# Optimization experiments

Hardware: AMD Instinct MI355X
Metric: run time of the kernel (lower is better)

Reference implementation:

```python
import jax, jax.numpy as jnp
import numpy as np

B, L, D, H, M = 2, 4096, 1024, 16, 256
DH = D // H
EPS = 1e-6
LN_EPS = 1e-5


def setup_inputs() -> dict:
    key = jax.random.key(0)
    ks = jax.random.split(key, 6)
    inp = {
        "x": jax.random.normal(ks[0], (B, L, D), jnp.float32),
        "Wq": jax.random.normal(ks[1], (D, D), jnp.float32) * (D ** -0.5),
        "Wk": jax.random.normal(ks[2], (D, D), jnp.float32) * (D ** -0.5),
        "Wv": jax.random.normal(ks[3], (D, D), jnp.float32) * (D ** -0.5),
        "Wo": jax.random.normal(ks[4], (D, D), jnp.float32) * (D ** -0.5),
        "proj": jax.random.normal(ks[5], (H, M, DH), jnp.float32),
        "ln_g": jnp.ones((D,), jnp.float32),
        "ln_b": jnp.zeros((D,), jnp.float32),
        "scale_factor": 2,
    }
    return inp


def _heads(t, W):
    b, l, _ = t.shape
    return (t @ W).reshape(b, l, H, DH).transpose(0, 2, 1, 3)  # bhld


def _favor_features(u, proj):
    # u: [B,H,L,DH] already scaled by d_head**-0.25; proj: [H,M,DH]
    dash = jnp.einsum("bhld,hmd->bhlm", u, proj)
    diag = 0.5 * jnp.sum(u * u, axis=-1, keepdims=True)  # [B,H,L,1]
    stab = jnp.max(dash, axis=-1, keepdims=True)
    return jnp.exp(dash - diag - stab) * (M ** -0.5)  # [B,H,L,M]


def reference(x, Wq, Wk, Wv, Wo, proj, ln_g, ln_b, scale_factor):
    b, l, d = x.shape
    # nearest-neighbor upsample along sequence (F.interpolate default mode)
    up = jnp.repeat(x, scale_factor, axis=1)  # [B, L*s, D]

    scale = DH ** -0.25
    q = _heads(up, Wq) * scale   # [B,H,Lq,DH]
    k = _heads(x, Wk) * scale    # [B,H,L,DH]
    v = _heads(x, Wv)            # [B,H,L,DH]

    qf = _favor_features(q, proj)  # [B,H,Lq,M]
    kf = _favor_features(k, proj)  # [B,H,L,M]

    kv = jnp.einsum("bhlm,bhld->bhmd", kf, v)          # [B,H,M,DH]
    k_sum = jnp.sum(kf, axis=2)                          # [B,H,M]
    z = 1.0 / (jnp.einsum("bhlm,bhm->bhl", qf, k_sum) + EPS)
    attn = jnp.einsum("bhlm,bhmd->bhld", qf, kv) * z[..., None]

    lq = attn.shape[2]
    y = attn.transpose(0, 2, 1, 3).reshape(b, lq, d) @ Wo
    y = jax.nn.gelu(y, approximate=False)

    mu = jnp.mean(y, axis=-1, keepdims=True)
    var = jnp.mean((y - mu) ** 2, axis=-1, keepdims=True)
    return (y - mu) * jax.lax.rsqrt(var + LN_EPS) * ln_g + ln_b
```

## Files before the change

kernel.cpp:

```cpp
#include <hip/hip_runtime.h>

static constexpr int kB  = 2;
static constexpr int kL  = 4096;
static constexpr int kD  = 1024;
static constexpr int kH  = 16;
static constexpr int kDH = 64;
static constexpr int kM  = 256;
static constexpr int kN  = kB * kL;
static constexpr float kScale    = 0.35355339059327373f;
static constexpr float kInvSqrtM = 0.0625f;
static constexpr float kEps   = 1e-6f;
static constexpr float kLnEps = 1e-5f;

typedef __attribute__((ext_vector_type(8))) short short8;
typedef __attribute__((ext_vector_type(4))) float f32x4;

__device__ __forceinline__ float bf2f(unsigned short h) {
  union { unsigned int u; float f; } c;
  c.u = ((unsigned int)h) << 16;
  return c.f;
}
__device__ __forceinline__ unsigned short f2bf(float f) {
  union { float f; unsigned int u; } c;
  c.f = f;
  unsigned int u = c.u;
  u += 0x7fffu + ((u >> 16) & 1u);
  return (unsigned short)(u >> 16);
}

__device__ __forceinline__ void gload_lds16(const unsigned short* g,
                                            unsigned short* l) {
  __builtin_amdgcn_global_load_lds(
      (const __attribute__((address_space(1))) unsigned int*)g,
      (__attribute__((address_space(3))) unsigned int*)l, 16, 0, 0);
}

__global__ __launch_bounds__(256) void cast_bf16_kernel(
    const float* __restrict__ in, unsigned short* __restrict__ out)
{
  const int i = blockIdx.x * 256 + threadIdx.x;
  float4 v = ((const float4*)in)[i];
  ushort4 o;
  o.x = f2bf(v.x); o.y = f2bf(v.y); o.z = f2bf(v.z); o.w = f2bf(v.w);
  ((ushort4*)out)[i] = o;
}

__global__ __launch_bounds__(256) void transpose_cast_kernel(
    const float* __restrict__ W, unsigned short* __restrict__ WT)
{
  __shared__ float tile[32][33];
  const int n0 = blockIdx.x * 32, k0 = blockIdx.y * 32;
  const int t = threadIdx.x, kk = t >> 5, nn = t & 31;
#pragma unroll
  for (int i = 0; i < 4; ++i)
    tile[kk + i * 8][nn] = W[(size_t)(k0 + kk + i * 8) * kD + n0 + nn];
  __syncthreads();
#pragma unroll
  for (int i = 0; i < 4; ++i)
    WT[(size_t)(n0 + kk + i * 8) * kD + k0 + nn] = f2bf(tile[nn][kk + i * 8]);
}

template <int OUT_MODE>
__global__ __launch_bounds__(256) void gemm_mfma(
    const unsigned short* __restrict__ A, const unsigned short* __restrict__ BT,
    void* __restrict__ Cout, float alpha)
{
  __shared__ unsigned short As[128 * 32];
  __shared__ unsigned short Bs[128 * 32];
  __shared__ unsigned short Tbuf[OUT_MODE == 2 ? 64 * 136 : 1];
  const int tid = threadIdx.x, lane = tid & 63, w = tid >> 6;
  const int q = lane >> 4, c = lane & 15;
  const int wr = (w >> 1) * 64, wc = (w & 1) * 64;
  const int row0 = blockIdx.y * 128, col0 = blockIdx.x * 128;
  const int lrow = lane >> 2, lcol = (lane & 3) * 8;

  f32x4 acc[4][4];
#pragma unroll
  for (int i = 0; i < 4; ++i)
#pragma unroll
    for (int j = 0; j < 4; ++j) acc[i][j] = (f32x4)0.f;

  for (int k0 = 0; k0 < kD; k0 += 32) {
#pragma unroll
    for (int i = 0; i < 2; ++i) {
      const int r0 = w * 32 + i * 16;
      gload_lds16(&A[(size_t)(row0 + r0 + lrow) * kD + k0 + lcol], &As[r0 * 32]);
      gload_lds16(&BT[(size_t)(col0 + r0 + lrow) * kD + k0 + lcol], &Bs[r0 * 32]);
    }
    __syncthreads();
    short8 av[4], bv[4];
#pragma unroll
    for (int i = 0; i < 4; ++i)
      av[i] = *(const short8*)&As[(wr + i * 16 + c) * 32 + q * 8];
#pragma unroll
    for (int j = 0; j < 4; ++j)
      bv[j] = *(const short8*)&Bs[(wc + j * 16 + c) * 32 + q * 8];
#pragma unroll
    for (int i = 0; i < 4; ++i)
#pragma unroll
      for (int j = 0; j < 4; ++j)
        acc[i][j] = __builtin_amdgcn_mfma_f32_16x16x32_bf16(
            av[i], bv[j], acc[i][j], 0, 0, 0);
    __syncthreads();
  }

  if (OUT_MODE != 2) {
#pragma unroll
    for (int i = 0; i < 4; ++i)
#pragma unroll
      for (int j = 0; j < 4; ++j)
#pragma unroll
        for (int r = 0; r < 4; ++r) {
          const int row = row0 + wr + i * 16 + q * 4 + r;
          const int col = col0 + wc + j * 16 + c;
          const float v = alpha * acc[i][j][r];
          if (OUT_MODE == 1)
            ((unsigned short*)Cout)[(size_t)row * kD + col] = f2bf(v);
          else
            ((float*)Cout)[(size_t)row * kD + col] = v;
        }
  } else {
    const int bq = row0 >> 12, l0 = row0 & 4095;
#pragma unroll
    for (int hh = 0; hh < 2; ++hh) {
      if ((w & 1) == hh) {
#pragma unroll
        for (int i = 0; i < 4; ++i)
#pragma unroll
          for (int j = 0; j < 4; ++j) {
            ushort4 o;
            o.x = f2bf(acc[i][j][0]); o.y = f2bf(acc[i][j][1]);
            o.z = f2bf(acc[i][j][2]); o.w = f2bf(acc[i][j][3]);
            *(ushort4*)&Tbuf[(j * 16 + c) * 136 + wr + i * 16 + q * 4] = o;
          }
      }
      __syncthreads();
      {
        const int dl = tid >> 2, seg = tid & 3;
        const size_t dst =
            ((size_t)(bq * 1024 + col0 + hh * 64 + dl)) * (size_t)kL +
            l0 + seg * 32;
        uint4* gp = (uint4*)((unsigned short*)Cout + dst);
        const unsigned short* sp = &Tbuf[dl * 136 + seg * 32];
#pragma unroll
        for (int u = 0; u < 4; ++u) gp[u] = *(const uint4*)&sp[u * 8];
      }
      __syncthreads();
    }
  }
}

template <int TRANS>
__global__ __launch_bounds__(256) void favor_mfma(
    const unsigned short* __restrict__ U, const unsigned short* __restrict__ projb,
    unsigned short* __restrict__ F)
{
  __shared__ unsigned short Us[128 * 72];
  __shared__ unsigned short Ps[256 * 72];
  __shared__ float diagp[256];
  __shared__ float diag[128];
  unsigned short* Tbuf = Us;
  const int bh = blockIdx.x, b = bh >> 4, h = bh & 15;
  const int l0 = blockIdx.y * 128;
  const int tid = threadIdx.x, lane = tid & 63, w = tid >> 6;
  const int q = lane >> 4, c = lane & 15;
  const int wr = w * 32;

#pragma unroll
  for (int it = 0; it < 4; ++it) {
    int idx = it * 256 + tid;
    int row = idx >> 3, col8 = idx & 7;
    *(uint4*)&Us[row * 72 + col8 * 8] =
        *(const uint4*)&U[((size_t)(b * kL + l0 + row)) * kD + h * kDH + col8 * 8];
  }
#pragma unroll
  for (int it = 0; it < 8; ++it) {
    int idx = it * 256 + tid;
    int row = idx >> 3, col8 = idx & 7;
    *(uint4*)&Ps[row * 72 + col8 * 8] =
        *(const uint4*)&projb[((size_t)(h * kM + row)) * kDH + col8 * 8];
  }
  __syncthreads();

  {
    int row = tid & 127, half = tid >> 7;
    const unsigned short* ur = &Us[row * 72 + half * 32];
    float s = 0.f;
#pragma unroll
    for (int d8 = 0; d8 < 4; ++d8) {
      uint4 raw = *(const uint4*)&ur[d8 * 8];
      const unsigned short* us = (const unsigned short*)&raw;
#pragma unroll
      for (int j = 0; j < 8; ++j) { float v = bf2f(us[j]); s = fmaf(v, v, s); }
    }
    diagp[half * 128 + row] = s;
  }

  f32x4 acc[2][16];
#pragma unroll
  for (int i = 0; i < 2; ++i)
#pragma unroll
    for (int j = 0; j < 16; ++j) acc[i][j] = (f32x4)0.f;

#pragma unroll
  for (int ks = 0; ks < 2; ++ks) {
    short8 av[2];
#pragma unroll
    for (int i = 0; i < 2; ++i)
      av[i] = *(const short8*)&Us[(wr + i * 16 + c) * 72 + ks * 32 + q * 8];
#pragma unroll
    for (int jb = 0; jb < 2; ++jb) {
      short8 bv[8];
#pragma unroll
      for (int jl = 0; jl < 8; ++jl)
        bv[jl] = *(const short8*)&Ps[((jb * 8 + jl) * 16 + c) * 72 + ks * 32 + q * 8];
#pragma unroll
      for (int jl = 0; jl < 8; ++jl)
#pragma unroll
        for (int i = 0; i < 2; ++i)
          acc[i][jb * 8 + jl] = __builtin_amdgcn_mfma_f32_16x16x32_bf16(
              av[i], bv[jl], acc[i][jb * 8 + jl], 0, 0, 0);
    }
  }

  __syncthreads();
  if (tid < 128) diag[tid] = 0.5f * (diagp[tid] + diagp[128 + tid]);
  __syncthreads();

#pragma unroll
  for (int i = 0; i < 2; ++i)
#pragma unroll
    for (int r = 0; r < 4; ++r) {
      const int lrow = wr + i * 16 + q * 4 + r;
      float mx = -3.4e38f;
#pragma unroll
      for (int j = 0; j < 16; ++j) mx = fmaxf(mx, acc[i][j][r]);
      mx = fmaxf(mx, __shfl_xor(mx, 1, 64));
      mx = fmaxf(mx, __shfl_xor(mx, 2, 64));
      mx = fmaxf(mx, __shfl_xor(mx, 4, 64));
      mx = fmaxf(mx, __shfl_xor(mx, 8, 64));
      const float base = diag[lrow] + mx;
      if (TRANS == 0) {
        const size_t gbase = ((size_t)bh * kL + (l0 + lrow)) * kM;
#pragma unroll
        for (int j = 0; j < 16; ++j)
          F[gbase + j * 16 + c] = f2bf(__expf(acc[i][j][r] - base) * kInvSqrtM);
      } else {
#pragma unroll
        for (int j = 0; j < 16; ++j)
          acc[i][j][r] = __expf(acc[i][j][r] - base) * kInvSqrtM;
      }
    }

  if (TRANS == 1) {
#pragma unroll
    for (int mc = 0; mc < 4; ++mc) {
      __syncthreads();
#pragma unroll
      for (int jl = 0; jl < 4; ++jl) {
        const int jj = mc * 4 + jl;
#pragma unroll
        for (int i = 0; i < 2; ++i) {
          ushort4 o;
          o.x = f2bf(acc[i][jj][0]); o.y = f2bf(acc[i][jj][1]);
          o.z = f2bf(acc[i][jj][2]); o.w = f2bf(acc[i][jj][3]);
          *(ushort4*)&Tbuf[(jl * 16 + c) * 136 + wr + i * 16 + q * 4] = o;
        }
      }
      __syncthreads();
#pragma unroll
      for (int it = 0; it < 4; ++it) {
        int idx = it * 256 + tid;
        int row = idx >> 4, col8 = idx & 15;
        *(uint4*)&F[((size_t)(bh * kM + mc * 64 + row)) * (size_t)kL +
                    l0 + col8 * 8] = *(const uint4*)&Tbuf[row * 136 + col8 * 8];
      }
    }
  }
}

__global__ __launch_bounds__(256) void kv_mfma(
    const unsigned short* __restrict__ KFT, const unsigned short* __restrict__ VT,
    float* __restrict__ KVP, float* __restrict__ KSP)
{
  __shared__ unsigned short As[128 * 40];
  __shared__ unsigned short Bs[64 * 40];
  const int bh = blockIdx.x, mtile = blockIdx.y, split = blockIdx.z;
  const int tid = threadIdx.x, lane = tid & 63, w = tid >> 6;
  const int q = lane >> 4, c = lane & 15;
  const int l0 = split * 512;
  const unsigned short* Abase = KFT + ((size_t)(bh * kM + mtile * 128)) * kL + l0;
  const unsigned short* Bbase = VT + ((size_t)(bh * kDH)) * kL + l0;

  f32x4 acc[2][4];
#pragma unroll
  for (int i = 0; i < 2; ++i)
#pragma unroll
    for (int j = 0; j < 4; ++j) acc[i][j] = (f32x4)0.f;
  float ksr[2] = {0.f, 0.f};

  for (int k0 = 0; k0 < 512; k0 += 32) {
    __syncthreads();
#pragma unroll
    for (int it = 0; it < 2; ++it) {
      int idx = it * 256 + tid;
      int row = idx >> 2, c8 = (idx & 3) * 8;
      *(uint4*)&As[row * 40 + c8] = *(const uint4*)&Abase[(size_t)row * kL + k0 + c8];
    }
    {
      int row = tid >> 2, c8 = (tid & 3) * 8;
      *(uint4*)&Bs[row * 40 + c8] = *(const uint4*)&Bbase[(size_t)row * kL + k0 + c8];
    }
    __syncthreads();
    short8 av[2], bv[4];
#pragma unroll
    for (int i = 0; i < 2; ++i) {
      av[i] = *(const short8*)&As[(w * 32 + i * 16 + c) * 40 + q * 8];
#pragma unroll
      for (int e = 0; e < 8; ++e) ksr[i] += bf2f((unsigned short)av[i][e]);
    }
#pragma unroll
    for (int j = 0; j < 4; ++j)
      bv[j] = *(const short8*)&Bs[(j * 16 + c) * 40 + q * 8];
#pragma unroll
    for (int i = 0; i < 2; ++i)
#pragma unroll
      for (int j = 0; j < 4; ++j)
        acc[i][j] = __builtin_amdgcn_mfma_f32_16x16x32_bf16(
            av[i], bv[j], acc[i][j], 0, 0, 0);
  }

  const int blk = (bh * 2 + mtile) * 8 + split;
  float* op = KVP + (size_t)blk * (128 * 64);
#pragma unroll
  for (int i = 0; i < 2; ++i)
#pragma unroll
    for (int j = 0; j < 4; ++j)
#pragma unroll
      for (int r = 0; r < 4; ++r)
        op[(w * 32 + i * 16 + q * 4 + r) * 64 + j * 16 + c] = acc[i][j][r];

#pragma unroll
  for (int i = 0; i < 2; ++i) {
    float s = ksr[i];
    s += __shfl_xor(s, 16, 64);
    s += __shfl_xor(s, 32, 64);
    if (q == 0) KSP[blk * 128 + w * 32 + i * 16 + c] = s;
  }
}

__global__ __launch_bounds__(256) void kv_reduce_kernel(
    const float* __restrict__ KVP, const float* __restrict__ KSP,
    unsigned short* __restrict__ KVT)
{
  const int blk = blockIdx.x;
  const int bh = blk / 80, n = blk - bh * 80;
  const int t = threadIdx.x;
  const int mt = t >> 7, ml = t & 127;
  float s = 0.f;
  if (n < 64) {
#pragma unroll
    for (int sp = 0; sp < 8; ++sp)
      s += KVP[((size_t)((bh * 2 + mt) * 8 + sp)) * (128 * 64) + ml * 64 + n];
  } else if (n == 64) {
#pragma unroll
    for (int sp = 0; sp < 8; ++sp)
      s += KSP[((bh * 2 + mt) * 8 + sp) * 128 + ml];
  }
  KVT[(size_t)bh * (80 * kM) + n * kM + t] = f2bf(s);
}

__global__ __launch_bounds__(256) void attn_mfma(
    const unsigned short* __restrict__ QF, const unsigned short* __restrict__ KVT,
    unsigned short* __restrict__ ATTN)
{
  __shared__ unsigned short kvs[80 * 264];
  __shared__ unsigned short qs[128 * 40];
  const int bh = blockIdx.x, b = bh >> 4, h = bh & 15;
  const int l0 = blockIdx.y * 128;
  const int tid = threadIdx.x, lane = tid & 63, w = tid >> 6;
  const int q = lane >> 4, c = lane & 15;
  const int trow = tid >> 2, tc8 = (tid & 3) * 8;

#pragma unroll
  for (int it = 0; it < 20; ++it) {
    int idx4 = it * 256 + tid;
    int row = idx4 >> 6, col4 = idx4 & 63;
    *(ushort4*)&kvs[row * 264 + col4 * 4] =
        *(const ushort4*)&KVT[(size_t)bh * (80 * kM) + row * kM + col4 * 4];
  }

  f32x4 acc[2][5];
#pragma unroll
  for (int i = 0; i < 2; ++i)
#pragma unroll
    for (int j = 0; j < 5; ++j) acc[i][j] = (f32x4)0.f;

  for (int kk = 0; kk < 8; ++kk) {
    __syncthreads();
#pragma unroll
    for (int i = 0; i < 2; ++i)
      *(uint4*)&qs[(trow + 64 * i) * 40 + tc8] =
          *(const uint4*)&QF[((size_t)bh * kL + (l0 + trow + 64 * i)) * kM +
                             kk * 32 + tc8];
    __syncthreads();
    short8 bv[5];
#pragma unroll
    for (int j = 0; j < 5; ++j)
      bv[j] = *(const short8*)&kvs[(j * 16 + c) * 264 + kk * 32 + q * 8];
#pragma unroll
    for (int i = 0; i < 2; ++i) {
      short8 av = *(const short8*)&qs[(w * 32 + i * 16 + c) * 40 + q * 8];
#pragma unroll
      for (int j = 0; j < 5; ++j)
        acc[i][j] = __builtin_amdgcn_mfma_f32_16x16x32_bf16(
            av, bv[j], acc[i][j], 0, 0, 0);
    }
  }

#pragma unroll
  for (int i = 0; i < 2; ++i)
#pragma unroll
    for (int r = 0; r < 4; ++r) {
      float den = __shfl(acc[i][4][r], (lane & 48));
      float z = 1.f / (den + kEps);
      const int row = l0 + w * 32 + i * 16 + q * 4 + r;
      const size_t base = ((size_t)(b * kL + row)) * kD + h * kDH;
#pragma unroll
      for (int j = 0; j < 4; ++j)
        ATTN[base + j * 16 + c] = f2bf(acc[i][j][r] * z);
    }
}

__global__ __launch_bounds__(256) void gelu_ln_kernel(
    const float* __restrict__ Y, const float* __restrict__ lng,
    const float* __restrict__ lnb, float* __restrict__ OUT)
{
  __shared__ float r1[4], r2[4];
  const int n = blockIdx.x;
  const int tid = threadIdx.x, lane = tid & 63, w = tid >> 6;

  float4 y4 = ((const float4*)(Y + (size_t)n * kD))[tid];
  float g0 = 0.5f * y4.x * (1.f + erff(y4.x * 0.70710678118654752f));
  float g1 = 0.5f * y4.y * (1.f + erff(y4.y * 0.70710678118654752f));
  float g2 = 0.5f * y4.z * (1.f + erff(y4.z * 0.70710678118654752f));
  float g3 = 0.5f * y4.w * (1.f + erff(y4.w * 0.70710678118654752f));

  float s  = (g0 + g1) + (g2 + g3);
  float ss = (g0 * g0 + g1 * g1) + (g2 * g2 + g3 * g3);
#pragma unroll
  for (int off = 32; off; off >>= 1) {
    s  += __shfl_xor(s, off, 64);
    ss += __shfl_xor(ss, off, 64);
  }
  if (lane == 0) { r1[w] = s; r2[w] = ss; }
  __syncthreads();
  s  = (r1[0] + r1[1]) + (r1[2] + r1[3]);
  ss = (r2[0] + r2[1]) + (r2[2] + r2[3]);
  float mu  = s * (1.f / (float)kD);
  float var = ss * (1.f / (float)kD) - mu * mu;
  float inv = rsqrtf(var + kLnEps);

  float4 gg = ((const float4*)lng)[tid];
  float4 bb = ((const float4*)lnb)[tid];
  float4 o;
  o.x = (g0 - mu) * inv * gg.x + bb.x;
  o.y = (g1 - mu) * inv * gg.y + bb.y;
  o.z = (g2 - mu) * inv * gg.z + bb.z;
  o.w = (g3 - mu) * inv * gg.w + bb.w;

  const int b = n >> 12, l = n & 4095;
  const int cc = tid * 4;
  size_t base = ((size_t)(b * 8192 + 2 * l)) * kD + cc;
  *(float4*)(OUT + base)      = o;
  *(float4*)(OUT + base + kD) = o;
}

extern "C" void kernel_launch(void* const* d_in, const int* in_sizes, int n_in,
                              void* d_out, int out_size, void* d_ws, size_t ws_size,
                              hipStream_t stream)
{
  (void)in_sizes; (void)n_in; (void)out_size; (void)ws_size;
  const float* x    = (const float*)d_in[0];
  const float* Wq   = (const float*)d_in[1];
  const float* Wk   = (const float*)d_in[2];
  const float* Wv   = (const float*)d_in[3];
  const float* Wo   = (const float*)d_in[4];
  const float* proj = (const float*)d_in[5];
  const float* lng  = (const float*)d_in[6];
  const float* lnb  = (const float*)d_in[7];
  float* out = (float*)d_out;

  char* ws = (char*)d_ws;
  const size_t MB = 1024 * 1024;
  unsigned short* xb  = (unsigned short*)(ws);
  unsigned short* WqT = (unsigned short*)(ws + 16 * MB);
  unsigned short* WkT = (unsigned short*)(ws + 18 * MB);
  unsigned short* WvT = (unsigned short*)(ws + 20 * MB);
  unsigned short* WoT = (unsigned short*)(ws + 22 * MB);
  unsigned short* Qb  = (unsigned short*)(ws + 24 * MB);
  unsigned short* Kb  = (unsigned short*)(ws + 40 * MB);
  unsigned short* VT  = (unsigned short*)(ws + 56 * MB);
  unsigned short* QF  = (unsigned short*)(ws + 72 * MB);
  unsigned short* KFT = (unsigned short*)(ws + 136 * MB);
  float* KSP          = (float*)(ws + 200 * MB);
  unsigned short* KVT = (unsigned short*)(ws + 201 * MB);
  unsigned short* projb = (unsigned short*)(ws + 203 * MB);
  float* KVP          = (float*)(ws + 24 * MB);
  unsigned short* ATTN = Kb;
  float* Y            = (float*)(ws + 72 * MB);

  cast_bf16_kernel<<<(kN * kD) / 1024, 256, 0, stream>>>(x, xb);
  cast_bf16_kernel<<<(kH * kM * kDH) / 1024, 256, 0, stream>>>(proj, projb);
  transpose_cast_kernel<<<dim3(32, 32), 256, 0, stream>>>(Wq, WqT);
  transpose_cast_kernel<<<dim3(32, 32), 256, 0, stream>>>(Wk, WkT);
  transpose_cast_kernel<<<dim3(32, 32), 256, 0, stream>>>(Wv, WvT);
  transpose_cast_kernel<<<dim3(32, 32), 256, 0, stream>>>(Wo, WoT);

  dim3 gg(8, 64);
  gemm_mfma<1><<<gg, 256, 0, stream>>>(xb, WkT, Kb, kScale);
  gemm_mfma<2><<<gg, 256, 0, stream>>>(xb, WvT, VT, 1.0f);
  gemm_mfma<1><<<gg, 256, 0, stream>>>(xb, WqT, Qb, kScale);

  favor_mfma<0><<<dim3(32, 32), 256, 0, stream>>>(Qb, projb, QF);
  favor_mfma<1><<<dim3(32, 32), 256, 0, stream>>>(Kb, projb, KFT);

  kv_mfma<<<dim3(32, 2, 8), 256, 0, stream>>>(KFT, VT, KVP, KSP);
  kv_reduce_kernel<<<32 * 80, 256, 0, stream>>>(KVP, KSP, KVT);

  attn_mfma<<<dim3(32, 32), 256, 0, stream>>>(QF, KVT, ATTN);

  gemm_mfma<0><<<gg, 256, 0, stream>>>(ATTN, WoT, Y, 1.0f);

  gelu_ln_kernel<<<kN, 256, 0, stream>>>(Y, lng, lnb, out);
}
```

Before: 371.4 us.

## Fuse key feature map with KV and k-sum reduction using atomics

```diff
diff --git a/kernel.cpp b/kernel.cpp
--- a/kernel.cpp
+++ b/kernel.cpp
@@ -45,10 +45,20 @@
   ((ushort4*)out)[i] = o;
 }
 
-__global__ __launch_bounds__(256) void transpose_cast_kernel(
-    const float* __restrict__ W, unsigned short* __restrict__ WT)
+__global__ __launch_bounds__(256) void zero_f32_kernel(float* __restrict__ p)
+{
+  ((float4*)p)[blockIdx.x * 256 + threadIdx.x] = make_float4(0.f, 0.f, 0.f, 0.f);
+}
+
+__global__ __launch_bounds__(256) void transpose_cast4_kernel(
+    const float* __restrict__ W0, const float* __restrict__ W1,
+    const float* __restrict__ W2, const float* __restrict__ W3,
+    unsigned short* __restrict__ WqkvT, unsigned short* __restrict__ WoT)
 {
   __shared__ float tile[32][33];
+  const int z = blockIdx.z;
+  const float* W = (z == 0) ? W0 : (z == 1) ? W1 : (z == 2) ? W2 : W3;
+  unsigned short* WT = (z < 3) ? (WqkvT + (size_t)z * kD * kD) : WoT;
   const int n0 = blockIdx.x * 32, k0 = blockIdx.y * 32;
   const int t = threadIdx.x, kk = t >> 5, nn = t & 31;
 #pragma unroll
@@ -150,8 +160,7 @@
   }
 }
 
-template <int TRANS>
-__global__ __launch_bounds__(256) void favor_mfma(
+__global__ __launch_bounds__(256) void favor_q_mfma(
     const unsigned short* __restrict__ U, const unsigned short* __restrict__ projb,
     unsigned short* __restrict__ F)
 {
@@ -159,7 +168,6 @@
   __shared__ unsigned short Ps[256 * 72];
   __shared__ float diagp[256];
   __shared__ float diag[128];
-  unsigned short* Tbuf = Us;
   const int bh = blockIdx.x, b = bh >> 4, h = bh & 15;
   const int l0 = blockIdx.y * 128;
   const int tid = threadIdx.x, lane = tid & 63, w = tid >> 6;
@@ -240,133 +248,175 @@
       mx = fmaxf(mx, __shfl_xor(mx, 4, 64));
       mx = fmaxf(mx, __shfl_xor(mx, 8, 64));
       const float base = diag[lrow] + mx;
-      if (TRANS == 0) {
-        const size_t gbase = ((size_t)bh * kL + (l0 + lrow)) * kM;
-#pragma unroll
-        for (int j = 0; j < 16; ++j)
-          F[gbase + j * 16 + c] = f2bf(__expf(acc[i][j][r] - base) * kInvSqrtM);
-      } else {
-#pragma unroll
-        for (int j = 0; j < 16; ++j)
-          acc[i][j][r] = __expf(acc[i][j][r] - base) * kInvSqrtM;
-      }
-    }
-
-  if (TRANS == 1) {
-#pragma unroll
-    for (int mc = 0; mc < 4; ++mc) {
-      __syncthreads();
-#pragma unroll
-      for (int jl = 0; jl < 4; ++jl) {
-        const int jj = mc * 4 + jl;
-#pragma unroll
-        for (int i = 0; i < 2; ++i) {
-          ushort4 o;
-          o.x = f2bf(acc[i][jj][0]); o.y = f2bf(acc[i][jj][1]);
-          o.z = f2bf(acc[i][jj][2]); o.w = f2bf(acc[i][jj][3]);
-          *(ushort4*)&Tbuf[(jl * 16 + c) * 136 + wr + i * 16 + q * 4] = o;
-        }
-      }
-      __syncthreads();
-#pragma unroll
-      for (int it = 0; it < 4; ++it) {
-        int idx = it * 256 + tid;
-        int row = idx >> 4, col8 = idx & 15;
-        *(uint4*)&F[((size_t)(bh * kM + mc * 64 + row)) * (size_t)kL +
-                    l0 + col8 * 8] = *(const uint4*)&Tbuf[row * 136 + col8 * 8];
-      }
-    }
-  }
-}
-
-__global__ __launch_bounds__(256) void kv_mfma(
-    const unsigned short* __restrict__ KFT, const unsigned short* __restrict__ VT,
-    float* __restrict__ KVP, float* __restrict__ KSP)
-{
-  __shared__ unsigned short As[128 * 40];
-  __shared__ unsigned short Bs[64 * 40];
-  const int bh = blockIdx.x, mtile = blockIdx.y, split = blockIdx.z;
+      const size_t gbase = ((size_t)bh * kL + (l0 + lrow)) * kM;
+#pragma unroll
+      for (int j = 0; j < 16; ++j)
+        F[gbase + j * 16 + c] = f2bf(__expf(acc[i][j][r] - base) * kInvSqrtM);
+    }
+}
+
+__global__ __launch_bounds__(256) void favor_k_fused(
+    const unsigned short* __restrict__ U, const unsigned short* __restrict__ projb,
+    const unsigned short* __restrict__ VT, float* __restrict__ KVF,
+    float* __restrict__ KSF)
+{
+  __shared__ unsigned short Us[128 * 72];
+  __shared__ unsigned short Ps[256 * 72];
+  __shared__ float diagp[256];
+  __shared__ float diag[128];
+  unsigned short* Tbuf = Us;
+  unsigned short* Vs   = Ps;
+  const int bh = blockIdx.x, b = bh >> 4, h = bh & 15;
+  const int l0 = blockIdx.y * 128;
   const int tid = threadIdx.x, lane = tid & 63, w = tid >> 6;
   const int q = lane >> 4, c = lane & 15;
-  const int l0 = split * 512;
-  const unsigned short* Abase = KFT + ((size_t)(bh * kM + mtile * 128)) * kL + l0;
-  const unsigned short* Bbase = VT + ((size_t)(bh * kDH)) * kL + l0;
-
-  f32x4 acc[2][4];
+  const int wr = w * 32;
+
+#pragma unroll
+  for (int it = 0; it < 4; ++it) {
+    int idx = it * 256 + tid;
+    int row = idx >> 3, col8 = idx & 7;
+    *(uint4*)&Us[row * 72 + col8 * 8] =
+        *(const uint4*)&U[((size_t)(b * kL + l0 + row)) * kD + h * kDH + col8 * 8];
+  }
+#pragma unroll
+  for (int it = 0; it < 8; ++it) {
+    int idx = it * 256 + tid;
+    int row = idx >> 3, col8 = idx & 7;
+    *(uint4*)&Ps[row * 72 + col8 * 8] =
+        *(const uint4*)&projb[((size_t)(h * kM + row)) * kDH + col8 * 8];
+  }
+  __syncthreads();
+
+  {
+    int row = tid & 127, half = tid >> 7;
+    const unsigned short* ur = &Us[row * 72 + half * 32];
+    float s = 0.f;
+#pragma unroll
+    for (int d8 = 0; d8 < 4; ++d8) {
+      uint4 raw = *(const uint4*)&ur[d8 * 8];
+      const unsigned short* us = (const unsigned short*)&raw;
+#pragma unroll
+      for (int j = 0; j < 8; ++j) { float v = bf2f(us[j]); s = fmaf(v, v, s); }
+    }
+    diagp[half * 128 + row] = s;
+  }
+
+  f32x4 acc[2][16];
 #pragma unroll
   for (int i = 0; i < 2; ++i)
 #pragma unroll
-    for (int j = 0; j < 4; ++j) acc[i][j] = (f32x4)0.f;
-  float ksr[2] = {0.f, 0.f};
-
-  for (int k0 = 0; k0 < 512; k0 += 32) {
-    __syncthreads();
-#pragma unroll
-    for (int it = 0; it < 2; ++it) {
-      int idx = it * 256 + tid;
-      int row = idx >> 2, c8 = (idx & 3) * 8;
-      *(uint4*)&As[row * 40 + c8] = *(const uint4*)&Abase[(size_t)row * kL + k0 + c8];
-    }
-    {
-      int row = tid >> 2, c8 = (tid & 3) * 8;
-      *(uint4*)&Bs[row * 40 + c8] = *(const uint4*)&Bbase[(size_t)row * kL + k0 + c8];
-    }
-    __syncthreads();
-    short8 av[2], bv[4];
-#pragma unroll
-    for (int i = 0; i < 2; ++i) {
-      av[i] = *(const short8*)&As[(w * 32 + i * 16 + c) * 40 + q * 8];
-#pragma unroll
-      for (int e = 0; e < 8; ++e) ksr[i] += bf2f((unsigned short)av[i][e]);
-    }
-#pragma unroll
-    for (int j = 0; j < 4; ++j)
-      bv[j] = *(const short8*)&Bs[(j * 16 + c) * 40 + q * 8];
+    for (int j = 0; j < 16; ++j) acc[i][j] = (f32x4)0.f;
+
+#pragma unroll
+  for (int ks = 0; ks < 2; ++ks) {
+    short8 av[2];
 #pragma unroll
     for (int i = 0; i < 2; ++i)
-#pragma unroll
-      for (int j = 0; j < 4; ++j)
-        acc[i][j] = __builtin_amdgcn_mfma_f32_16x16x32_bf16(
-            av[i], bv[j], acc[i][j], 0, 0, 0);
-  }
-
-  const int blk = (bh * 2 + mtile) * 8 + split;
-  float* op = KVP + (size_t)blk * (128 * 64);
+      av[i] = *(const short8*)&Us[(wr + i * 16 + c) * 72 + ks * 32 + q * 8];
+#pragma unroll
+    for (int jb = 0; jb < 2; ++jb) {
+      short8 bv[8];
+#pragma unroll
+      for (int jl = 0; jl < 8; ++jl)
+        bv[jl] = *(const short8*)&Ps[((jb * 8 + jl) * 16 + c) * 72 + ks * 32 + q * 8];
+#pragma unroll
+      for (int jl = 0; jl < 8; ++jl)
+#pragma unroll
+        for (int i = 0; i < 2; ++i)
+          acc[i][jb * 8 + jl] = __builtin_amdgcn_mfma_f32_16x16x32_bf16(
+              av[i], bv[jl], acc[i][jb * 8 + jl], 0, 0, 0);
+    }
+  }
+
+  __syncthreads();
+
+#pragma unroll
+  for (int it = 0; it < 4; ++it) {
+    int idx = it * 256 + tid;
+    int row = idx >> 4, col8 = idx & 15;
+    *(uint4*)&Vs[row * 136 + col8 * 8] =
+        *(const uint4*)&VT[((size_t)(bh * kDH + row)) * (size_t)kL + l0 + col8 * 8];
+  }
+  if (tid < 128) diag[tid] = 0.5f * (diagp[tid] + diagp[128 + tid]);
+  __syncthreads();
+
 #pragma unroll
   for (int i = 0; i < 2; ++i)
 #pragma unroll
-    for (int j = 0; j < 4; ++j)
-#pragma unroll
-      for (int r = 0; r < 4; ++r)
-        op[(w * 32 + i * 16 + q * 4 + r) * 64 + j * 16 + c] = acc[i][j][r];
-
-#pragma unroll
-  for (int i = 0; i < 2; ++i) {
-    float s = ksr[i];
+    for (int r = 0; r < 4; ++r) {
+      const int lrow = wr + i * 16 + q * 4 + r;
+      float mx = -3.4e38f;
+#pragma unroll
+      for (int j = 0; j < 16; ++j) mx = fmaxf(mx, acc[i][j][r]);
+      mx = fmaxf(mx, __shfl_xor(mx, 1, 64));
+      mx = fmaxf(mx, __shfl_xor(mx, 2, 64));
+      mx = fmaxf(mx, __shfl_xor(mx, 4, 64));
+      mx = fmaxf(mx, __shfl_xor(mx, 8, 64));
+      const float base = diag[lrow] + mx;
+#pragma unroll
+      for (int j = 0; j < 16; ++j)
+        acc[i][j][r] = __expf(acc[i][j][r] - base) * kInvSqrtM;
+    }
+
+#pragma unroll
+  for (int j = 0; j < 16; ++j) {
+    float s = 0.f;
+#pragma unroll
+    for (int i = 0; i < 2; ++i)
+#pragma unroll
+      for (int r = 0; r < 4; ++r) s += acc[i][j][r];
     s += __shfl_xor(s, 16, 64);
     s += __shfl_xor(s, 32, 64);
-    if (q == 0) KSP[blk * 128 + w * 32 + i * 16 + c] = s;
-  }
-}
-
-__global__ __launch_bounds__(256) void kv_reduce_kernel(
-    const float* __restrict__ KVP, const float* __restrict__ KSP,
+    if (q == 0) atomicAdd(&KSF[bh * kM + j * 16 + c], s);
+  }
+
+#pragma unroll
+  for (int mc = 0; mc < 4; ++mc) {
+    __syncthreads();
+#pragma unroll
+    for (int jl = 0; jl < 4; ++jl) {
+      const int jj = mc * 4 + jl;
+#pragma unroll
+      for (int i = 0; i < 2; ++i) {
+        ushort4 o;
+        o.x = f2bf(acc[i][jj][0]); o.y = f2bf(acc[i][jj][1]);
+        o.z = f2bf(acc[i][jj][2]); o.w = f2bf(acc[i][jj][3]);
+        *(ushort4*)&Tbuf[(jl * 16 + c) * 136 + wr + i * 16 + q * 4] = o;
+      }
+    }
+    __syncthreads();
+    f32x4 kvacc[4];
+#pragma unroll
+    for (int mj = 0; mj < 4; ++mj) kvacc[mj] = (f32x4)0.f;
+#pragma unroll
+    for (int ks = 0; ks < 4; ++ks) {
+      const short8 av = *(const short8*)&Vs[(w * 16 + c) * 136 + ks * 32 + q * 8];
+#pragma unroll
+      for (int mj = 0; mj < 4; ++mj) {
+        const short8 bv = *(const short8*)&Tbuf[(mj * 16 + c) * 136 + ks * 32 + q * 8];
+        kvacc[mj] = __builtin_amdgcn_mfma_f32_16x16x32_bf16(av, bv, kvacc[mj], 0, 0, 0);
+      }
+    }
+#pragma unroll
+    for (int mj = 0; mj < 4; ++mj)
+#pragma unroll
+      for (int r = 0; r < 4; ++r)
+        atomicAdd(&KVF[((size_t)(bh * kDH + w * 16 + q * 4 + r)) * kM +
+                       mc * 64 + mj * 16 + c], kvacc[mj][r]);
+  }
+}
+
+__global__ __launch_bounds__(256) void kvf_to_kvt(
+    const float* __restrict__ KVF, const float* __restrict__ KSF,
     unsigned short* __restrict__ KVT)
 {
   const int blk = blockIdx.x;
   const int bh = blk / 80, n = blk - bh * 80;
   const int t = threadIdx.x;
-  const int mt = t >> 7, ml = t & 127;
   float s = 0.f;
-  if (n < 64) {
-#pragma unroll
-    for (int sp = 0; sp < 8; ++sp)
-      s += KVP[((size_t)((bh * 2 + mt) * 8 + sp)) * (128 * 64) + ml * 64 + n];
-  } else if (n == 64) {
-#pragma unroll
-    for (int sp = 0; sp < 8; ++sp)
-      s += KSP[((bh * 2 + mt) * 8 + sp) * 128 + ml];
-  }
+  if (n < 64)       s = KVF[((size_t)(bh * kDH + n)) * kM + t];
+  else if (n == 64) s = KSF[bh * kM + t];
   KVT[(size_t)bh * (80 * kM) + n * kM + t] = f2bf(s);
 }
 
@@ -493,40 +543,37 @@
 
   char* ws = (char*)d_ws;
   const size_t MB = 1024 * 1024;
-  unsigned short* xb  = (unsigned short*)(ws);
-  unsigned short* WqT = (unsigned short*)(ws + 16 * MB);
-  unsigned short* WkT = (unsigned short*)(ws + 18 * MB);
-  unsigned short* WvT = (unsigned short*)(ws + 20 * MB);
-  unsigned short* WoT = (unsigned short*)(ws + 22 * MB);
-  unsigned short* Qb  = (unsigned short*)(ws + 24 * MB);
-  unsigned short* Kb  = (unsigned short*)(ws + 40 * MB);
-  unsigned short* VT  = (unsigned short*)(ws + 56 * MB);
-  unsigned short* QF  = (unsigned short*)(ws + 72 * MB);
-  unsigned short* KFT = (unsigned short*)(ws + 136 * MB);
-  float* KSP          = (float*)(ws + 200 * MB);
-  unsigned short* KVT = (unsigned short*)(ws + 201 * MB);
+  unsigned short* xb    = (unsigned short*)(ws);
+  unsigned short* WqkvT = (unsigned short*)(ws + 16 * MB);
+  unsigned short* WoT   = (unsigned short*)(ws + 22 * MB);
+  unsigned short* Qb    = (unsigned short*)(ws + 24 * MB);
+  unsigned short* Kb    = (unsigned short*)(ws + 40 * MB);
+  unsigned short* VT    = (unsigned short*)(ws + 56 * MB);
+  unsigned short* QF    = (unsigned short*)(ws + 72 * MB);
+  float* KVF            = (float*)(ws + 136 * MB);
+  float* KSF            = (float*)(ws + 138 * MB);
+  unsigned short* KVT   = (unsigned short*)(ws + 201 * MB);
   unsigned short* projb = (unsigned short*)(ws + 203 * MB);
-  float* KVP          = (float*)(ws + 24 * MB);
-  unsigned short* ATTN = Kb;
-  float* Y            = (float*)(ws + 72 * MB);
+  unsigned short* ATTN  = Kb;
+  float* Y              = (float*)(ws + 72 * MB);
+  unsigned short* WqT = WqkvT;
+  unsigned short* WkT = WqkvT + (size_t)kD * kD;
+  unsigned short* WvT = WqkvT + (size_t)2 * kD * kD;
 
   cast_bf16_kernel<<<(kN * kD) / 1024, 256, 0, stream>>>(x, xb);
   cast_bf16_kernel<<<(kH * kM * kDH) / 1024, 256, 0, stream>>>(proj, projb);
-  transpose_cast_kernel<<<dim3(32, 32), 256, 0, stream>>>(Wq, WqT);
-  transpose_cast_kernel<<<dim3(32, 32), 256, 0, stream>>>(Wk, WkT);
-  transpose_cast_kernel<<<dim3(32, 32), 256, 0, stream>>>(Wv, WvT);
-  transpose_cast_kernel<<<dim3(32, 32), 256, 0, stream>>>(Wo, WoT);
+  transpose_cast4_kernel<<<dim3(32, 32, 4), 256, 0, stream>>>(
+      Wq, Wk, Wv, Wo, WqkvT, WoT);
+  zero_f32_kernel<<<520, 256, 0, stream>>>(KVF);
 
   dim3 gg(8, 64);
   gemm_mfma<1><<<gg, 256, 0, stream>>>(xb, WkT, Kb, kScale);
   gemm_mfma<2><<<gg, 256, 0, stream>>>(xb, WvT, VT, 1.0f);
+  favor_k_fused<<<dim3(32, 32), 256, 0, stream>>>(Kb, projb, VT, KVF, KSF);
+  kvf_to_kvt<<<32 * 80, 256, 0, stream>>>(KVF, KSF, KVT);
+
   gemm_mfma<1><<<gg, 256, 0, stream>>>(xb, WqT, Qb, kScale);
-
-  favor_mfma<0><<<dim3(32, 32), 256, 0, stream>>>(Qb, projb, QF);
-  favor_mfma<1><<<dim3(32, 32), 256, 0, stream>>>(Kb, projb, KFT);
-
-  kv_mfma<<<dim3(32, 2, 8), 256, 0, stream>>>(KFT, VT, KVP, KSP);
-  kv_reduce_kernel<<<32 * 80, 256, 0, stream>>>(KVP, KSP, KVT);
+  favor_q_mfma<<<dim3(32, 32), 256, 0, stream>>>(Qb, projb, QF);
 
   attn_mfma<<<dim3(32, 32), 256, 0, stream>>>(QF, KVT, ATTN);
 
```

New measurement: 376.3 us. No clear change (+1.3%).
